# Optimization experiments

Hardware: AMD Instinct MI355X
Metric: run time of the kernel (lower is better)

## Reference

```python
import jax, jax.numpy as jnp
import numpy as np

N_NODES = 100000
N_EDGES = 1000000
IN_DIM = 64
OUT_DIM = 64


def setup_inputs() -> dict:
    key = jax.random.key(0)
    k1, k2, k3 = jax.random.split(key, 3)
    x = jax.random.normal(k1, (N_NODES, IN_DIM), dtype=jnp.float32)
    edge_index = jax.random.randint(k2, (2, N_EDGES), 0, N_NODES, dtype=jnp.int64)
    # PyG GCNConv linear weight [out_dim, in_dim] (glorot-ish scale) and bias
    W = jax.random.normal(k3, (OUT_DIM, IN_DIM), dtype=jnp.float32) * (1.0 / np.sqrt(IN_DIM))
    b = jnp.zeros((OUT_DIM,), dtype=jnp.float32)
    return {"x": x, "edge_index": edge_index, "W": W, "b": b}


def reference(x, edge_index, W, b):
    # GCNConv: add self-loops, symmetric deg^{-1/2} normalization,
    # linear transform, scatter-add aggregation, bias.
    # Dropout is identity in eval mode.
    N = x.shape[0]
    loop = jnp.arange(N, dtype=edge_index.dtype)
    src = jnp.concatenate([edge_index[0], loop])  # [E+N]
    dst = jnp.concatenate([edge_index[1], loop])  # [E+N]

    deg = jax.ops.segment_sum(jnp.ones_like(dst, dtype=x.dtype), dst, num_segments=N)
    dinv = jnp.where(deg > 0, jax.lax.rsqrt(deg), 0.0)  # [N]
    norm = dinv[src] * dinv[dst]                         # [E+N]

    h = x @ W.T                                          # [N, out_dim]
    msg = h[src] * norm[:, None]                         # gather + scale
    out = jax.ops.segment_sum(msg, dst, num_segments=N)  # scatter-add
    return out + b
```

## Files before the change

kernel.cpp:

```cpp
#include <hip/hip_runtime.h>

#define DIM 64
#define BIN_SHIFT 7
#define NODES_PER_BIN 128
#define MAX_BINS 1024
#define BIN_CAP 2048
#define CHUNK_EDGES 2048
#define SCATTER_THREADS 512
#define GEMM_ROWS 128
#define FXSCALE 65536.0f
#define FXINV (1.0f / 65536.0f)
#define FXBIAS 524288u
#define MAGIC 12582912.0f
#define MAGIC_I 0x4B400000u
#define ACC_U64 33


using bf16x8 = __attribute__((ext_vector_type(8))) short;
using f32x4  = __attribute__((ext_vector_type(4))) float;

__device__ __forceinline__ unsigned short f2bf(float f) {
    unsigned u = __float_as_uint(f);
    u += 0x7fffu + ((u >> 16) & 1u);
    return (unsigned short)(u >> 16);
}
__device__ __forceinline__ float bf2f(unsigned short u) {
    return __uint_as_float((unsigned)u << 16);
}

__global__ __launch_bounds__(SCATTER_THREADS) void bin_scatter_kernel(
    const void* __restrict__ ei, int* __restrict__ gcur,
    int* __restrict__ pairs, int E, int nbins) {
    __shared__ int h1[MAX_BINS];
    __shared__ int base[MAX_BINS];
    __shared__ int s_notz;
    int tid = threadIdx.x;
    if (tid == 0) s_notz = 0;
    for (int i = tid; i < nbins; i += SCATTER_THREADS) h1[i] = 0;
    __syncthreads();
    if (((const int*)ei)[2 * tid + 1] != 0) s_notz = 1;
    __syncthreads();
    int is64 = (s_notz == 0);
    int chunk = blockIdx.x * CHUNK_EDGES;

    int ss[CHUNK_EDGES / SCATTER_THREADS], dd[CHUNK_EDGES / SCATTER_THREADS];
#pragma unroll
    for (int k = 0; k < CHUNK_EDGES / SCATTER_THREADS; ++k) {
        int i = chunk + k * SCATTER_THREADS + tid;
        if (i < E) {
            int s, d;
            if (is64) {
                s = (int)((const long long*)ei)[i];
                d = (int)((const long long*)ei)[(long long)i + E];
            } else {
                s = ((const int*)ei)[i];
                d = ((const int*)ei)[i + E];
            }
            ss[k] = s; dd[k] = d;
            atomicAdd(&h1[d >> BIN_SHIFT], 1);
        } else {
            dd[k] = -1;
        }
    }
    __syncthreads();
    for (int i = tid; i < nbins; i += SCATTER_THREADS) {
        int c = h1[i];
        base[i] = c ? (i * BIN_CAP + atomicAdd(&gcur[i], c)) : 0;
        h1[i] = 0;
    }
    __syncthreads();
#pragma unroll
    for (int k = 0; k < CHUNK_EDGES / SCATTER_THREADS; ++k) {
        if (dd[k] >= 0) {
            int bin = dd[k] >> BIN_SHIFT;
            int r = atomicAdd(&h1[bin], 1);
            int pos = base[bin] + r;
            if (pos < (bin + 1) * BIN_CAP)
                pairs[pos] = (ss[k] << BIN_SHIFT) | (dd[k] & (NODES_PER_BIN - 1));
        }
    }
}

__global__ __launch_bounds__(256) void degree_kernel(const int* __restrict__ pairs,
                                                     const int* __restrict__ gcur,
                                                     int* __restrict__ deg,
                                                     float* __restrict__ dinv, int N) {
    __shared__ int sdeg[NODES_PER_BIN];
    int b = blockIdx.x;
    int tid = threadIdx.x;
    int base = b * BIN_CAP;
    int cnt = min(gcur[b], BIN_CAP);
    int node0 = b << BIN_SHIFT;
    int nn = min(NODES_PER_BIN, N - node0);
    if (tid < NODES_PER_BIN) sdeg[tid] = 0;
    __syncthreads();
    for (int i = tid; i < cnt; i += 256)
        atomicAdd(&sdeg[pairs[base + i] & (NODES_PER_BIN - 1)], 1);
    __syncthreads();
    if (tid < nn) {
        int d = sdeg[tid];
        deg[node0 + tid] = d;
        dinv[node0 + tid] = rsqrtf((float)(d + 1));
    }
}

__global__ __launch_bounds__(256) void gemm_kernel(const float* __restrict__ x,
                                                   const float* __restrict__ W,
                                                   const float* __restrict__ dinv,
                                                   unsigned short* __restrict__ h, int N) {
    __shared__ unsigned short Xs[GEMM_ROWS * 64];
    __shared__ unsigned short Ws[64 * 64];
    __shared__ float sdinv[GEMM_ROWS];
    int tid = threadIdx.x;
    int row0 = blockIdx.x * GEMM_ROWS;
    int nn = min(GEMM_ROWS, N - row0);

#pragma unroll
    for (int u = 0; u < 2; ++u) {
        int idx = u * 256 + tid;
        int c = idx >> 3, k0 = (idx & 7) * 8;
        float4 a = *(const float4*)&W[c * 64 + k0];
        float4 b = *(const float4*)&W[c * 64 + k0 + 4];
        bf16x8 v;
        v[0] = (short)f2bf(a.x); v[1] = (short)f2bf(a.y);
        v[2] = (short)f2bf(a.z); v[3] = (short)f2bf(a.w);
        v[4] = (short)f2bf(b.x); v[5] = (short)f2bf(b.y);
        v[6] = (short)f2bf(b.z); v[7] = (short)f2bf(b.w);
        int byteoff = c * 128 + ((k0 * 2) ^ ((c & 7) << 4));
        *(bf16x8*)((char*)Ws + byteoff) = v;
    }
    const float* xbase = x + (size_t)row0 * DIM;
#pragma unroll
    for (int u = 0; u < 4; ++u) {
        int idx = u * 256 + tid;
        int r = idx >> 3, k0 = (idx & 7) * 8;
        float4 a = make_float4(0.f, 0.f, 0.f, 0.f), b = a;
        if (r < nn) {
            a = *(const float4*)&xbase[r * DIM + k0];
            b = *(const float4*)&xbase[r * DIM + k0 + 4];
        }
        bf16x8 v;
        v[0] = (short)f2bf(a.x); v[1] = (short)f2bf(a.y);
        v[2] = (short)f2bf(a.z); v[3] = (short)f2bf(a.w);
        v[4] = (short)f2bf(b.x); v[5] = (short)f2bf(b.y);
        v[6] = (short)f2bf(b.z); v[7] = (short)f2bf(b.w);
        int byteoff = r * 128 + ((k0 * 2) ^ ((r & 7) << 4));
        *(bf16x8*)((char*)Xs + byteoff) = v;
    }
    if (tid < GEMM_ROWS) sdinv[tid] = (tid < nn) ? dinv[row0 + tid] : 0.0f;
    __syncthreads();

    int w = tid >> 6, l = tid & 63;
    int lm = l & 15, kg = l >> 4;
    f32x4 acc[2][4] = {};
#pragma unroll
    for (int ks = 0; ks < 2; ++ks) {
        int kbyte = ks * 64 + kg * 16;
        int r0g = 32 * w + lm;
        int r1g = 32 * w + 16 + lm;
        bf16x8 a0 = *(const bf16x8*)((const char*)Xs + r0g * 128 + (kbyte ^ ((r0g & 7) << 4)));
        bf16x8 a1 = *(const bf16x8*)((const char*)Xs + r1g * 128 + (kbyte ^ ((r1g & 7) << 4)));
#pragma unroll
        for (int nt = 0; nt < 4; ++nt) {
            int ng = nt * 16 + lm;
            bf16x8 bv = *(const bf16x8*)((const char*)Ws + ng * 128 + (kbyte ^ ((ng & 7) << 4)));
            acc[0][nt] = __builtin_amdgcn_mfma_f32_16x16x32_bf16(a0, bv, acc[0][nt], 0, 0, 0);
            acc[1][nt] = __builtin_amdgcn_mfma_f32_16x16x32_bf16(a1, bv, acc[1][nt], 0, 0, 0);
        }
    }
#pragma unroll
    for (int mt = 0; mt < 2; ++mt) {
#pragma unroll
        for (int j = 0; j < 4; ++j) {
            int rl = 32 * w + 16 * mt + (l >> 4) * 4 + j;
            if (rl < nn) {
                float dv = sdinv[rl];
                size_t rowoff = (size_t)(row0 + rl) * DIM;
#pragma unroll
                for (int nt = 0; nt < 4; ++nt)
                    h[rowoff + nt * 16 + lm] = f2bf(acc[mt][nt][j] * dv);
            }
        }
    }
}

__global__ __launch_bounds__(512) void aggregate_kernel(
    const unsigned short* __restrict__ h, const int* __restrict__ pairs,
    const int* __restrict__ gcur, const int* __restrict__ deg,
    const float* __restrict__ dinv, const float* __restrict__ bias,
    float* __restrict__ out, int N) {
    __shared__ unsigned long long acc[NODES_PER_BIN * ACC_U64];
    int b = blockIdx.x;
    int tid = threadIdx.x;
    int cnt = min(gcur[b], BIN_CAP);
    int node0 = b << BIN_SHIFT;
    int nn = min(NODES_PER_BIN, N - node0);

    for (int i = tid; i < NODES_PER_BIN * ACC_U64; i += 512) acc[i] = 0ULL;
    __syncthreads();

    int wave = tid >> 6, lane = tid & 63;
    int g = lane >> 4;
    int fq = lane & 15;
    const int* pb = pairs + b * BIN_CAP;
    int dummy = N << BIN_SHIFT;

    for (int j0 = 32 * wave; j0 < cnt; j0 += 256) {
        int pk[8]; bool vd[8];
#pragma unroll
        for (int u = 0; u < 8; ++u) {
            int e = j0 + 4 * u + g;
            vd[u] = (e < cnt);
            pk[u] = vd[u] ? pb[e] : dummy;
        }
        ushort4 r[8];
#pragma unroll
        for (int u = 0; u < 8; ++u)
            r[u] = *(const ushort4*)(h + (size_t)(pk[u] >> BIN_SHIFT) * DIM + 4 * fq);
#pragma unroll
        for (int u = 0; u < 8; ++u) {
            unsigned q0 = __float_as_uint(fmaf(bf2f(r[u].x), FXSCALE, MAGIC)) - (MAGIC_I - FXBIAS);
            unsigned q1 = __float_as_uint(fmaf(bf2f(r[u].y), FXSCALE, MAGIC)) - (MAGIC_I - FXBIAS);
            unsigned q2 = __float_as_uint(fmaf(bf2f(r[u].z), FXSCALE, MAGIC)) - (MAGIC_I - FXBIAS);
            unsigned q3 = __float_as_uint(fmaf(bf2f(r[u].w), FXSCALE, MAGIC)) - (MAGIC_I - FXBIAS);
            if (vd[u]) {
                unsigned long long* ar =
                    &acc[(pk[u] & (NODES_PER_BIN - 1)) * ACC_U64 + 2 * fq];
                atomicAdd(&ar[0], (unsigned long long)q0 | ((unsigned long long)q1 << 32));
                atomicAdd(&ar[1], (unsigned long long)q2 | ((unsigned long long)q3 << 32));
            }
        }
    }
    __syncthreads();

    const int* accd = (const int*)acc;
    float bl = bias[lane];
    for (int n0 = wave; n0 < nn; n0 += 8) {
        int gn = node0 + n0;
        int dgn = deg[gn];
        float di = dinv[gn];
        unsigned q = (unsigned)accd[n0 * (2 * ACC_U64) + lane];
        int sfx = (int)(q - (unsigned)dgn * FXBIAS);
        float sum = (float)sfx * FXINV;
        float self = bf2f(h[(size_t)gn * DIM + lane]);
        out[(size_t)gn * DIM + lane] = (sum + self) * di + bl;
    }
}

extern "C" void kernel_launch(void* const* d_in, const int* in_sizes, int n_in,
                              void* d_out, int out_size, void* d_ws, size_t ws_size,
                              hipStream_t stream) {
    const float* x = (const float*)d_in[0];
    const void* ei = d_in[1];
    const float* W = (const float*)d_in[2];
    const float* b = (const float*)d_in[3];
    float* out = (float*)d_out;

    int N = in_sizes[0] / DIM;
    int E = in_sizes[1] / 2;
    int nbins = (N + NODES_PER_BIN - 1) >> BIN_SHIFT;

    char* ws = (char*)d_ws;
    auto align256 = [](size_t v) { return (v + 255) & ~(size_t)255; };
    size_t off = 0;
    int* gcur = (int*)(ws + off);              off = align256(off + (size_t)MAX_BINS * 4);
    int* deg  = (int*)(ws + off);              off = align256(off + (size_t)(N + 1) * 4);
    float* dinv = (float*)(ws + off);          off = align256(off + (size_t)(N + 1) * 4);
    int* pairs = (int*)(ws + off);             off = align256(off + ((size_t)nbins * BIN_CAP + 64) * 4);
    unsigned short* h = (unsigned short*)(ws + off); off = align256(off + (size_t)(N + 1) * DIM * 2);

    int nchunks = (E + CHUNK_EDGES - 1) / CHUNK_EDGES;
    int gemmblocks = (N + GEMM_ROWS - 1) / GEMM_ROWS;

    hipMemsetAsync(gcur, 0, (size_t)MAX_BINS * 4, stream);
    bin_scatter_kernel<<<nchunks, SCATTER_THREADS, 0, stream>>>(ei, gcur, pairs, E, nbins);
    degree_kernel<<<nbins, 256, 0, stream>>>(pairs, gcur, deg, dinv, N);
    gemm_kernel<<<gemmblocks, 256, 0, stream>>>(x, W, dinv, h, N);
    aggregate_kernel<<<nbins, 512, 0, stream>>>(h, pairs, gcur, deg, dinv, b, out, N);
}
```

Measured before the change: 134.6 us.

## Fuse degree computation into GEMM kernel and enlarge scatter chunks

Merges the per-bin degree counting kernel into the GEMM kernel, since GEMM row blocks and degree bins both cover 128 nodes, which removes one kernel launch and the dinv round trip through global memory. The scatter kernel now handles 4096 edges per block with 1024 threads, so fewer blocks are launched and there are fewer global atomics on bin cursors. The GEMM blocks now also read the pair lists, which lengthens each block, and the larger scatter blocks may lower occupancy.

```diff
diff --git a/kernel.cpp b/kernel.cpp
--- a/kernel.cpp
+++ b/kernel.cpp
@@ -5,8 +5,8 @@
 #define NODES_PER_BIN 128
 #define MAX_BINS 1024
 #define BIN_CAP 2048
-#define CHUNK_EDGES 2048
-#define SCATTER_THREADS 512
+#define CHUNK_EDGES 4096
+#define SCATTER_THREADS 1024
 #define GEMM_ROWS 128
 #define FXSCALE 65536.0f
 #define FXINV (1.0f / 65536.0f)
@@ -81,51 +81,33 @@
     }
 }
 
-__global__ __launch_bounds__(256) void degree_kernel(const int* __restrict__ pairs,
-                                                     const int* __restrict__ gcur,
-                                                     int* __restrict__ deg,
-                                                     float* __restrict__ dinv, int N) {
-    __shared__ int sdeg[NODES_PER_BIN];
-    int b = blockIdx.x;
-    int tid = threadIdx.x;
-    int base = b * BIN_CAP;
-    int cnt = min(gcur[b], BIN_CAP);
-    int node0 = b << BIN_SHIFT;
-    int nn = min(NODES_PER_BIN, N - node0);
-    if (tid < NODES_PER_BIN) sdeg[tid] = 0;
-    __syncthreads();
-    for (int i = tid; i < cnt; i += 256)
-        atomicAdd(&sdeg[pairs[base + i] & (NODES_PER_BIN - 1)], 1);
-    __syncthreads();
-    if (tid < nn) {
-        int d = sdeg[tid];
-        deg[node0 + tid] = d;
-        dinv[node0 + tid] = rsqrtf((float)(d + 1));
-    }
-}
-
-__global__ __launch_bounds__(256) void gemm_kernel(const float* __restrict__ x,
-                                                   const float* __restrict__ W,
-                                                   const float* __restrict__ dinv,
-                                                   unsigned short* __restrict__ h, int N) {
+__global__ __launch_bounds__(256) void deg_gemm_kernel(
+    const float* __restrict__ x, const float* __restrict__ W,
+    const int* __restrict__ pairs, const int* __restrict__ gcur,
+    int* __restrict__ deg, float* __restrict__ dinv,
+    unsigned short* __restrict__ h, int N) {
     __shared__ unsigned short Xs[GEMM_ROWS * 64];
     __shared__ unsigned short Ws[64 * 64];
-    __shared__ float sdinv[GEMM_ROWS];
+    __shared__ int sdeg[NODES_PER_BIN];
+    __shared__ float sdinv[NODES_PER_BIN];
     int tid = threadIdx.x;
-    int row0 = blockIdx.x * GEMM_ROWS;
+    int b = blockIdx.x;
+    int row0 = b << BIN_SHIFT;
     int nn = min(GEMM_ROWS, N - row0);
-
+    int cntb = min(gcur[b], BIN_CAP);
+
+    if (tid < NODES_PER_BIN) sdeg[tid] = 0;
 #pragma unroll
     for (int u = 0; u < 2; ++u) {
         int idx = u * 256 + tid;
         int c = idx >> 3, k0 = (idx & 7) * 8;
         float4 a = *(const float4*)&W[c * 64 + k0];
-        float4 b = *(const float4*)&W[c * 64 + k0 + 4];
+        float4 bb = *(const float4*)&W[c * 64 + k0 + 4];
         bf16x8 v;
         v[0] = (short)f2bf(a.x); v[1] = (short)f2bf(a.y);
         v[2] = (short)f2bf(a.z); v[3] = (short)f2bf(a.w);
-        v[4] = (short)f2bf(b.x); v[5] = (short)f2bf(b.y);
-        v[6] = (short)f2bf(b.z); v[7] = (short)f2bf(b.w);
+        v[4] = (short)f2bf(bb.x); v[5] = (short)f2bf(bb.y);
+        v[6] = (short)f2bf(bb.z); v[7] = (short)f2bf(bb.w);
         int byteoff = c * 128 + ((k0 * 2) ^ ((c & 7) << 4));
         *(bf16x8*)((char*)Ws + byteoff) = v;
     }
@@ -134,20 +116,33 @@
     for (int u = 0; u < 4; ++u) {
         int idx = u * 256 + tid;
         int r = idx >> 3, k0 = (idx & 7) * 8;
-        float4 a = make_float4(0.f, 0.f, 0.f, 0.f), b = a;
+        float4 a = make_float4(0.f, 0.f, 0.f, 0.f), bb = a;
         if (r < nn) {
             a = *(const float4*)&xbase[r * DIM + k0];
-            b = *(const float4*)&xbase[r * DIM + k0 + 4];
+            bb = *(const float4*)&xbase[r * DIM + k0 + 4];
         }
         bf16x8 v;
         v[0] = (short)f2bf(a.x); v[1] = (short)f2bf(a.y);
         v[2] = (short)f2bf(a.z); v[3] = (short)f2bf(a.w);
-        v[4] = (short)f2bf(b.x); v[5] = (short)f2bf(b.y);
-        v[6] = (short)f2bf(b.z); v[7] = (short)f2bf(b.w);
+        v[4] = (short)f2bf(bb.x); v[5] = (short)f2bf(bb.y);
+        v[6] = (short)f2bf(bb.z); v[7] = (short)f2bf(bb.w);
         int byteoff = r * 128 + ((k0 * 2) ^ ((r & 7) << 4));
         *(bf16x8*)((char*)Xs + byteoff) = v;
     }
-    if (tid < GEMM_ROWS) sdinv[tid] = (tid < nn) ? dinv[row0 + tid] : 0.0f;
+    __syncthreads();
+    const int* pb = pairs + b * BIN_CAP;
+    for (int i = tid; i < cntb; i += 256)
+        atomicAdd(&sdeg[pb[i] & (NODES_PER_BIN - 1)], 1);
+    __syncthreads();
+    if (tid < NODES_PER_BIN) {
+        int d = sdeg[tid];
+        float dv = rsqrtf((float)(d + 1));
+        sdinv[tid] = dv;
+        if (tid < nn) {
+            deg[row0 + tid] = d;
+            dinv[row0 + tid] = dv;
+        }
+    }
     __syncthreads();
 
     int w = tid >> 6, l = tid & 63;
@@ -270,11 +265,10 @@
     unsigned short* h = (unsigned short*)(ws + off); off = align256(off + (size_t)(N + 1) * DIM * 2);
 
     int nchunks = (E + CHUNK_EDGES - 1) / CHUNK_EDGES;
-    int gemmblocks = (N + GEMM_ROWS - 1) / GEMM_ROWS;
+    int gemmblocks = nbins;
 
     hipMemsetAsync(gcur, 0, (size_t)MAX_BINS * 4, stream);
     bin_scatter_kernel<<<nchunks, SCATTER_THREADS, 0, stream>>>(ei, gcur, pairs, E, nbins);
-    degree_kernel<<<nbins, 256, 0, stream>>>(pairs, gcur, deg, dinv, N);
-    gemm_kernel<<<gemmblocks, 256, 0, stream>>>(x, W, dinv, h, N);
+    deg_gemm_kernel<<<gemmblocks, 256, 0, stream>>>(x, W, pairs, gcur, deg, dinv, h, N);
     aggregate_kernel<<<nbins, 512, 0, stream>>>(h, pairs, gcur, deg, dinv, b, out, N);
 }
```

New measurement: 128.6 us. 4.5% less time.
